# Kernel optimization log

Hardware: AMD Instinct MI355X
Metric: run time of the kernel (lower is better)

## Reference

```python
import jax, jax.numpy as jnp
import numpy as np
from jax.scipy.stats import norm

B, T = 64, 1024
RNN_DIM, EMB_DIM, ATTN_DIM = 1024, 512, 128
N_FILT, KSIZE, N_MEAN = 32, 31, 8
LOGVAR_MIN = float(np.log(0.1 ** 2))
LOGVAR_MAX = float(np.log(36.77 ** 2))


def setup_inputs() -> dict:
    key = jax.random.key(0)
    ks = jax.random.split(key, 10)
    return {
        "attention_hidden_state": jax.random.normal(ks[0], (B, RNN_DIM), jnp.float32),
        "memory": jax.random.normal(ks[1], (B, T, EMB_DIM), jnp.float32),
        "processed_memory": jax.random.normal(ks[2], (B, T, ATTN_DIM), jnp.float32),
        "attention_weights_cat": jax.random.uniform(ks[3], (B, 2, T), jnp.float32),
        "prev_means": jnp.zeros((B,), jnp.float32),
        "mask": jnp.zeros((B, T), bool),
        # learned parameters (all Linear layers bias=False; conv bias=False)
        "W_query": jax.random.normal(ks[4], (ATTN_DIM, RNN_DIM), jnp.float32) * 0.02,
        "conv_w": jax.random.normal(ks[5], (N_FILT, 2, KSIZE), jnp.float32) * 0.1,
        "W_loc": jax.random.normal(ks[6], (ATTN_DIM, N_FILT), jnp.float32) * 0.1,
        "W_mean": jax.random.normal(ks[7], (N_MEAN, ATTN_DIM), jnp.float32) * 0.05,
        "W_logvar": jax.random.normal(ks[8], (1, ATTN_DIM), jnp.float32) * 0.05,
    }


def reference(attention_hidden_state, memory, processed_memory, attention_weights_cat,
              prev_means, mask, W_query, conv_w, W_loc, W_mean, W_logvar):
    pad = (KSIZE - 1) // 2
    # query projection: [B, 1, attn_dim]
    processed_query = (attention_hidden_state @ W_query.T)[:, None, :]
    # location layer: conv1d(2 -> n_filters, same padding) then dense -> [B, T, attn_dim]
    loc = jax.lax.conv_general_dilated(
        attention_weights_cat, conv_w, window_strides=(1,),
        padding=[(pad, pad)], dimension_numbers=("NCH", "OIH", "NCH"))  # [B, F, T]
    processed_loc = jnp.einsum("bft,df->btd", loc, W_loc)
    pred = jnp.tanh(processed_query + processed_loc + processed_memory)  # [B, T, D]
    avg = pred.mean(axis=1)                                              # [B, D]
    # monotonic mean increment (soft_clip = softplus, keeps increments positive)
    mean_inc = jax.nn.softplus(avg @ W_mean.T).sum(axis=-1)              # [B]
    means = prev_means + mean_inc                                        # [B]
    logvars = (LOGVAR_MAX - LOGVAR_MIN) * jax.nn.sigmoid(avg @ W_logvar.T) + LOGVAR_MIN
    stds = jnp.exp(0.5 * logvars[:, 0])                                  # [B]
    # Gaussian window: CDF(x+0.5) - CDF(x-0.5), x = 0..T-1
    x = jnp.arange(T, dtype=jnp.float32)[None, :]                        # [1, T]
    mu, sd = means[:, None], stds[:, None]
    p = norm.cdf((x + 0.5 - mu) / sd) - norm.cdf((x - 0.5 - mu) / sd)    # [B, T]
    attention_weights = jnp.where(mask, 0.0, p)
    attention_context = jnp.einsum("bt,bte->be", attention_weights, memory)
    return attention_context, attention_weights
```

## Files before the change

### kernel.cpp

```cpp
#include <hip/hip_runtime.h>
#include <math.h>

#define B 64
#define T 1024
#define RNN_DIM 1024
#define EMB_DIM 512
#define ATTN_DIM 128
#define N_FILT 32
#define KSIZE 31
#define N_MEAN 8

#define LOGVAR_MIN (-4.605170185988091f)
#define LOGVAR_MAX (7.2093654f)

#define TTILE 256
#define AWWIN 288
#define MAGIC 0x73C0FFEEu

typedef __attribute__((ext_vector_type(8))) short bf16x8;
typedef __attribute__((ext_vector_type(4))) float f32x4;

__device__ __forceinline__ unsigned short f2bf(float x) {
    unsigned u = __float_as_uint(x);
    u += 0x7FFFu + ((u >> 16) & 1u);
    return (unsigned short)(u >> 16);
}

__global__ __launch_bounds__(512, 1) void fused_kernel(
        const float* __restrict__ hidden,
        const float* __restrict__ memory,
        const float* __restrict__ pm,
        const float* __restrict__ awcat,
        const float* __restrict__ prevm,
        const unsigned char* __restrict__ mask,
        const float* __restrict__ Wq,
        const float* __restrict__ convw,
        const float* __restrict__ Wloc,
        const float* __restrict__ Wmean,
        const float* __restrict__ Wlogvar,
        unsigned* __restrict__ pqflags,
        unsigned* __restrict__ avgflags,
        float* __restrict__ pq_ws,
        float* __restrict__ avg_part,
        float* __restrict__ out_ctx,
        float* __restrict__ out_w) {
    __shared__ __align__(16) float aw_s[2][AWWIN];
    __shared__ __align__(16) float pq_s[ATTN_DIM];
    __shared__ __align__(16) unsigned short loc_bf[TTILE * 32];
    __shared__ __align__(16) unsigned short wl_bf[ATTN_DIM * 32];
    __shared__ __align__(16) float red2[8][ATTN_DIM];
    __shared__ __align__(16) float a_s[ATTN_DIM];
    __shared__ float w_s[T];
    __shared__ __align__(16) float4 cred_s[16][32];
    __shared__ float musd_s[2];
    __shared__ int slo_s[8], shi_s[8];

    const int x = blockIdx.x;
    const int b = blockIdx.y;
    const int tid = threadIdx.x;
    const int t0 = x * TTILE;
    const int lane = tid & 63;
    const int w = tid >> 6;

    for (int idx = tid; idx < 2 * AWWIN; idx += 512) {
        int c = idx / AWWIN, j = idx - c * AWWIN;
        int tg = t0 - 16 + j;
        aw_s[c][j] = (tg >= 0 && tg < T) ? awcat[(size_t)b * 2 * T + c * T + tg] : 0.f;
    }

    {
        const float4* wsrc = (const float4*)Wloc;
        float4 v0 = wsrc[tid * 2], v1 = wsrc[tid * 2 + 1];
        uint4 pk;
        pk.x = (unsigned)f2bf(v0.x) | ((unsigned)f2bf(v0.y) << 16);
        pk.y = (unsigned)f2bf(v0.z) | ((unsigned)f2bf(v0.w) << 16);
        pk.z = (unsigned)f2bf(v1.x) | ((unsigned)f2bf(v1.y) << 16);
        pk.w = (unsigned)f2bf(v1.z) | ((unsigned)f2bf(v1.w) << 16);
        *(uint4*)&wl_bf[tid * 8] = pk;
    }

    {
        const float4* h4 = (const float4*)(hidden + (size_t)b * RNN_DIM);
        float4 hv0 = h4[lane], hv1 = h4[lane + 64];
        float4 hv2 = h4[lane + 128], hv3 = h4[lane + 192];
#pragma unroll
        for (int pass = 0; pass < 4; ++pass) {
            int d = x * 32 + pass * 8 + w;
            const float4* w4 = (const float4*)(Wq + (size_t)d * RNN_DIM);
            float4 wa = w4[lane], wb = w4[lane + 64];
            float4 wc = w4[lane + 128], wd = w4[lane + 192];
            float acc = hv0.x * wa.x + hv0.y * wa.y + hv0.z * wa.z + hv0.w * wa.w;
            acc += hv1.x * wb.x + hv1.y * wb.y + hv1.z * wb.z + hv1.w * wb.w;
            acc += hv2.x * wc.x + hv2.y * wc.y + hv2.z * wc.z + hv2.w * wc.w;
            acc += hv3.x * wd.x + hv3.y * wd.y + hv3.z * wd.z + hv3.w * wd.w;
#pragma unroll
            for (int off = 32; off > 0; off >>= 1)
                acc += __shfl_xor(acc, off, 64);
            if (lane == 0)
                __hip_atomic_store(&pq_ws[b * ATTN_DIM + d], acc,
                                   __ATOMIC_RELAXED, __HIP_MEMORY_SCOPE_AGENT);
        }
        asm volatile("s_waitcnt vmcnt(0)" ::: "memory");
    }
    __syncthreads();
    if (tid == 0)
        __hip_atomic_store(&pqflags[b * 4 + x], MAGIC,
                           __ATOMIC_RELEASE, __HIP_MEMORY_SCOPE_AGENT);

    {
        int f = tid & 31, tg8 = tid >> 5;
        float cw0[KSIZE], cw1[KSIZE];
#pragma unroll
        for (int k = 0; k < KSIZE; ++k) {
            cw0[k] = convw[(f * 2 + 0) * KSIZE + k];
            cw1[k] = convw[(f * 2 + 1) * KSIZE + k];
        }
#pragma unroll
        for (int p = 0; p < 2; ++p) {
            int o = tg8 + 16 * p;
            float a0[40], a1[40];
#pragma unroll
            for (int j = 0; j < 10; ++j) {
                float4 v0 = *(const float4*)&aw_s[0][o * 8 + 4 * j];
                float4 v1 = *(const float4*)&aw_s[1][o * 8 + 4 * j];
                a0[4 * j] = v0.x; a0[4 * j + 1] = v0.y; a0[4 * j + 2] = v0.z; a0[4 * j + 3] = v0.w;
                a1[4 * j] = v1.x; a1[4 * j + 1] = v1.y; a1[4 * j + 2] = v1.z; a1[4 * j + 3] = v1.w;
            }
#pragma unroll
            for (int i = 0; i < 8; ++i) {
                float s = 0.f;
#pragma unroll
                for (int k = 0; k < KSIZE; ++k)
                    s += a0[i + k + 1] * cw0[k] + a1[i + k + 1] * cw1[k];
                loc_bf[(o * 8 + i) * 32 + f] = f2bf(s);
            }
        }
    }
    __syncthreads();

    if (tid == 0) {
#pragma unroll
        for (int s = 0; s < 4; ++s) {
            const unsigned* fp = &pqflags[b * 4 + s];
            while (__hip_atomic_load(fp, __ATOMIC_RELAXED, __HIP_MEMORY_SCOPE_AGENT) != MAGIC)
                __builtin_amdgcn_s_sleep(1);
        }
    }
    __syncthreads();
    if (tid < ATTN_DIM)
        pq_s[tid] = __hip_atomic_load(&pq_ws[b * ATTN_DIM + tid],
                                      __ATOMIC_RELAXED, __HIP_MEMORY_SCOPE_AGENT);
    __syncthreads();

    {
        int col = lane & 15;
        int kg = lane >> 4;
        const float* pmL = pm + (size_t)(b * T + t0 + w * 32) * ATTN_DIM + col;

        float pmr[2][8][4];
#pragma unroll
        for (int m = 0; m < 2; ++m)
#pragma unroll
            for (int n = 0; n < 8; ++n)
#pragma unroll
                for (int j = 0; j < 4; ++j)
                    pmr[m][n][j] = pmL[(size_t)(m * 16 + kg * 4 + j) * ATTN_DIM + n * 16];

        bf16x8 bfrag[8];
#pragma unroll
        for (int n = 0; n < 8; ++n)
            bfrag[n] = *(const bf16x8*)&wl_bf[(n * 16 + col) * 32 + kg * 8];
        bf16x8 af[2];
#pragma unroll
        for (int m = 0; m < 2; ++m)
            af[m] = *(const bf16x8*)&loc_bf[(w * 32 + m * 16 + col) * 32 + kg * 8];
        float pqv[8];
#pragma unroll
        for (int n = 0; n < 8; ++n) pqv[n] = pq_s[n * 16 + col];

        float accs[8];
#pragma unroll
        for (int n = 0; n < 8; ++n) accs[n] = 0.f;
#pragma unroll
        for (int m = 0; m < 2; ++m) {
#pragma unroll
            for (int n = 0; n < 8; ++n) {
                f32x4 c = {0.f, 0.f, 0.f, 0.f};
                c = __builtin_amdgcn_mfma_f32_16x16x32_bf16(af[m], bfrag[n], c, 0, 0, 0);
#pragma unroll
                for (int j = 0; j < 4; ++j) {
                    float xv = c[j] + pqv[n] + pmr[m][n][j];
                    float e = __expf(2.f * xv);
                    accs[n] += 1.f - 2.f / (e + 1.f);
                }
            }
        }
#pragma unroll
        for (int n = 0; n < 8; ++n) {
            float s = accs[n];
            s += __shfl_xor(s, 16, 64);
            s += __shfl_xor(s, 32, 64);
            if (lane < 16) red2[w][n * 16 + lane] = s;
        }
    }
    __syncthreads();

    if (tid < ATTN_DIM) {
        float s = 0.f;
#pragma unroll
        for (int w2 = 0; w2 < 8; ++w2) s += red2[w2][tid];
        __hip_atomic_store(&avg_part[((size_t)b * 4 + x) * ATTN_DIM + tid], s,
                           __ATOMIC_RELAXED, __HIP_MEMORY_SCOPE_AGENT);
    }
    asm volatile("s_waitcnt vmcnt(0)" ::: "memory");
    __syncthreads();
    if (tid == 0) {
        __hip_atomic_store(&avgflags[b * 4 + x], MAGIC,
                           __ATOMIC_RELEASE, __HIP_MEMORY_SCOPE_AGENT);
#pragma unroll
        for (int s = 0; s < 4; ++s) {
            const unsigned* fp = &avgflags[b * 4 + s];
            while (__hip_atomic_load(fp, __ATOMIC_RELAXED, __HIP_MEMORY_SCOPE_AGENT) != MAGIC)
                __builtin_amdgcn_s_sleep(1);
        }
    }
    __syncthreads();

    if (tid < ATTN_DIM) {
        float s = 0.f;
#pragma unroll
        for (int ss = 0; ss < 4; ++ss)
            s += __hip_atomic_load(&avg_part[((size_t)b * 4 + ss) * ATTN_DIM + tid],
                                   __ATOMIC_RELAXED, __HIP_MEMORY_SCOPE_AGENT);
        a_s[tid] = s * (1.f / (float)T);
    }
    __syncthreads();

    if (tid < 64) {
        float macc[N_MEAN];
#pragma unroll
        for (int m = 0; m < N_MEAN; ++m) macc[m] = 0.f;
        float lv = 0.f;
#pragma unroll
        for (int i = 0; i < 2; ++i) {
            int d = tid + i * 64;
            float a = a_s[d];
#pragma unroll
            for (int m = 0; m < N_MEAN; ++m) macc[m] += a * Wmean[m * ATTN_DIM + d];
            lv += a * Wlogvar[d];
        }
#pragma unroll
        for (int off = 32; off > 0; off >>= 1) {
#pragma unroll
            for (int m = 0; m < N_MEAN; ++m) macc[m] += __shfl_xor(macc[m], off, 64);
            lv += __shfl_xor(lv, off, 64);
        }
        if (tid == 0) {
            float mean_inc = 0.f;
#pragma unroll
            for (int m = 0; m < N_MEAN; ++m) {
                float xx = macc[m];
                mean_inc += fmaxf(xx, 0.f) + log1pf(expf(-fabsf(xx)));
            }
            float mu = prevm[b] + mean_inc;
            float sig = 1.f / (1.f + expf(-lv));
            float logvar = (LOGVAR_MAX - LOGVAR_MIN) * sig + LOGVAR_MIN;
            musd_s[0] = mu;
            musd_s[1] = 1.f / expf(0.5f * logvar);
        }
    }
    __syncthreads();

    float mu = musd_s[0];
    float rsd = musd_s[1];
    const float is2 = 0.7071067811865476f;
    int lo = T, hi = -1;
#pragma unroll
    for (int r = 0; r < 2; ++r) {
        int t = tid + r * 512;
        float z1 = ((float)t + 0.5f - mu) * rsd * is2;
        float z2 = ((float)t - 0.5f - mu) * rsd * is2;
        float p = 0.5f * (erff(z1) - erff(z2));
        if (mask[(size_t)b * T + t]) p = 0.f;
        w_s[t] = p;
        if ((t >> 8) == x) out_w[(size_t)b * T + t] = p;
        if (p != 0.f) { lo = min(lo, t); hi = max(hi, t); }
    }
#pragma unroll
    for (int off = 32; off > 0; off >>= 1) {
        lo = min(lo, __shfl_xor(lo, off, 64));
        hi = max(hi, __shfl_xor(hi, off, 64));
    }
    if (lane == 0) { slo_s[w] = lo; shi_s[w] = hi; }
    __syncthreads();
#pragma unroll
    for (int wv = 0; wv < 8; ++wv) {
        lo = min(lo, slo_s[wv]);
        hi = max(hi, shi_s[wv]);
    }

    {
        int e4 = x * 32 + (tid & 31);
        int trow = tid >> 5;
        const float4* m4 = (const float4*)memory + (size_t)b * T * (EMB_DIM / 4);
        float4 acc = make_float4(0.f, 0.f, 0.f, 0.f);
        for (int t = lo + trow; t <= hi; t += 16) {
            float wvv = w_s[t];
            float4 mm = m4[(size_t)t * (EMB_DIM / 4) + e4];
            acc.x += wvv * mm.x;
            acc.y += wvv * mm.y;
            acc.z += wvv * mm.z;
            acc.w += wvv * mm.w;
        }
        if (trow != 0) cred_s[trow][tid & 31] = acc;
        __syncthreads();
        if (trow == 0) {
#pragma unroll
            for (int r = 1; r < 16; ++r) {
                float4 o = cred_s[r][tid & 31];
                acc.x += o.x; acc.y += o.y; acc.z += o.z; acc.w += o.w;
            }
            ((float4*)(out_ctx + (size_t)b * EMB_DIM))[e4] = acc;
        }
    }
}

extern "C" void kernel_launch(void* const* d_in, const int* in_sizes, int n_in,
                              void* d_out, int out_size, void* d_ws, size_t ws_size,
                              hipStream_t stream) {
    const float* hidden  = (const float*)d_in[0];
    const float* memory  = (const float*)d_in[1];
    const float* pm      = (const float*)d_in[2];
    const float* awcat   = (const float*)d_in[3];
    const float* prevm   = (const float*)d_in[4];
    const unsigned char* mask = (const unsigned char*)d_in[5];
    const float* Wq      = (const float*)d_in[6];
    const float* convw   = (const float*)d_in[7];
    const float* Wloc    = (const float*)d_in[8];
    const float* Wmean   = (const float*)d_in[9];
    const float* Wlogvar = (const float*)d_in[10];

    unsigned* pqflags  = (unsigned*)d_ws;
    unsigned* avgflags = pqflags + 256;
    float* pq_ws       = (float*)d_ws + 512;
    float* avg_part    = pq_ws + B * ATTN_DIM;

    float* out_ctx = (float*)d_out;
    float* out_w   = out_ctx + B * EMB_DIM;

    fused_kernel<<<dim3(4, B), 512, 0, stream>>>(
        hidden, memory, pm, awcat, prevm, mask, Wq, convw, Wloc, Wmean,
        Wlogvar, pqflags, avgflags, pq_ws, avg_part, out_ctx, out_w);
}
```

Baseline: 33.44 us.

## Split each batch over eight blocks of 128 timesteps instead of four

Doubles the grid to 8 blocks per batch row (512 total), each covering 128 timesteps, 16 query dims and 64 embedding columns. Launch bounds now allow 4 blocks per CU. The conv is restructured to process one channel at a time, which lowers register pressure. The pq flag wait is moved after the pm/fragment loads so the wait overlaps with memory traffic. The cross-block spin barriers now wait on 8 flags, and the context reduction becomes a tree. The goal is more parallelism and occupancy on the many-CU GPU. The cost is extra sync overhead and redundant per-block work such as the window computation and the W_loc conversion.

```diff
diff --git a/kernel.cpp b/kernel.cpp
--- a/kernel.cpp
+++ b/kernel.cpp
@@ -13,8 +13,9 @@
 #define LOGVAR_MIN (-4.605170185988091f)
 #define LOGVAR_MAX (7.2093654f)
 
-#define TTILE 256
-#define AWWIN 288
+#define NX 8
+#define TTILE 128
+#define AWWIN 160
 #define MAGIC 0x73C0FFEEu
 
 typedef __attribute__((ext_vector_type(8))) short bf16x8;
@@ -26,7 +27,7 @@
     return (unsigned short)(u >> 16);
 }
 
-__global__ __launch_bounds__(512, 1) void fused_kernel(
+__global__ __launch_bounds__(512, 4) void fused_kernel(
         const float* __restrict__ hidden,
         const float* __restrict__ memory,
         const float* __restrict__ pm,
@@ -51,12 +52,12 @@
     __shared__ __align__(16) float red2[8][ATTN_DIM];
     __shared__ __align__(16) float a_s[ATTN_DIM];
     __shared__ float w_s[T];
-    __shared__ __align__(16) float4 cred_s[16][32];
+    __shared__ __align__(16) float4 cred_s[32][16];
     __shared__ float musd_s[2];
     __shared__ int slo_s[8], shi_s[8];
 
-    const int x = blockIdx.x;
-    const int b = blockIdx.y;
+    const int b = blockIdx.x;
+    const int x = blockIdx.y;
     const int tid = threadIdx.x;
     const int t0 = x * TTILE;
     const int lane = tid & 63;
@@ -84,8 +85,8 @@
         float4 hv0 = h4[lane], hv1 = h4[lane + 64];
         float4 hv2 = h4[lane + 128], hv3 = h4[lane + 192];
 #pragma unroll
-        for (int pass = 0; pass < 4; ++pass) {
-            int d = x * 32 + pass * 8 + w;
+        for (int pass = 0; pass < 2; ++pass) {
+            int d = x * 16 + pass * 8 + w;
             const float4* w4 = (const float4*)(Wq + (size_t)d * RNN_DIM);
             float4 wa = w4[lane], wb = w4[lane + 64];
             float4 wc = w4[lane + 128], wd = w4[lane + 192];
@@ -104,76 +105,73 @@
     }
     __syncthreads();
     if (tid == 0)
-        __hip_atomic_store(&pqflags[b * 4 + x], MAGIC,
+        __hip_atomic_store(&pqflags[b * NX + x], MAGIC,
                            __ATOMIC_RELEASE, __HIP_MEMORY_SCOPE_AGENT);
 
     {
-        int f = tid & 31, tg8 = tid >> 5;
-        float cw0[KSIZE], cw1[KSIZE];
-#pragma unroll
-        for (int k = 0; k < KSIZE; ++k) {
-            cw0[k] = convw[(f * 2 + 0) * KSIZE + k];
-            cw1[k] = convw[(f * 2 + 1) * KSIZE + k];
-        }
-#pragma unroll
-        for (int p = 0; p < 2; ++p) {
-            int o = tg8 + 16 * p;
-            float a0[40], a1[40];
+        int f = tid & 31, o = tid >> 5;
+        float s[8];
+#pragma unroll
+        for (int i = 0; i < 8; ++i) s[i] = 0.f;
+#pragma unroll
+        for (int c = 0; c < 2; ++c) {
+            float cw[KSIZE];
+#pragma unroll
+            for (int k = 0; k < KSIZE; ++k)
+                cw[k] = convw[f * 2 * KSIZE + c * KSIZE + k];
+            float a[40];
 #pragma unroll
             for (int j = 0; j < 10; ++j) {
-                float4 v0 = *(const float4*)&aw_s[0][o * 8 + 4 * j];
-                float4 v1 = *(const float4*)&aw_s[1][o * 8 + 4 * j];
-                a0[4 * j] = v0.x; a0[4 * j + 1] = v0.y; a0[4 * j + 2] = v0.z; a0[4 * j + 3] = v0.w;
-                a1[4 * j] = v1.x; a1[4 * j + 1] = v1.y; a1[4 * j + 2] = v1.z; a1[4 * j + 3] = v1.w;
+                float4 v = *(const float4*)&aw_s[c][o * 8 + 4 * j];
+                a[4 * j] = v.x; a[4 * j + 1] = v.y; a[4 * j + 2] = v.z; a[4 * j + 3] = v.w;
             }
 #pragma unroll
             for (int i = 0; i < 8; ++i) {
-                float s = 0.f;
+                float t = 0.f;
 #pragma unroll
                 for (int k = 0; k < KSIZE; ++k)
-                    s += a0[i + k + 1] * cw0[k] + a1[i + k + 1] * cw1[k];
-                loc_bf[(o * 8 + i) * 32 + f] = f2bf(s);
-            }
-        }
-    }
-    __syncthreads();
-
-    if (tid == 0) {
-#pragma unroll
-        for (int s = 0; s < 4; ++s) {
-            const unsigned* fp = &pqflags[b * 4 + s];
-            while (__hip_atomic_load(fp, __ATOMIC_RELAXED, __HIP_MEMORY_SCOPE_AGENT) != MAGIC)
-                __builtin_amdgcn_s_sleep(1);
-        }
-    }
-    __syncthreads();
-    if (tid < ATTN_DIM)
-        pq_s[tid] = __hip_atomic_load(&pq_ws[b * ATTN_DIM + tid],
-                                      __ATOMIC_RELAXED, __HIP_MEMORY_SCOPE_AGENT);
+                    t += a[i + k + 1] * cw[k];
+                s[i] += t;
+            }
+        }
+#pragma unroll
+        for (int i = 0; i < 8; ++i)
+            loc_bf[(o * 8 + i) * 32 + f] = f2bf(s[i]);
+    }
     __syncthreads();
 
     {
         int col = lane & 15;
         int kg = lane >> 4;
-        const float* pmL = pm + (size_t)(b * T + t0 + w * 32) * ATTN_DIM + col;
-
-        float pmr[2][8][4];
-#pragma unroll
-        for (int m = 0; m < 2; ++m)
-#pragma unroll
-            for (int n = 0; n < 8; ++n)
-#pragma unroll
-                for (int j = 0; j < 4; ++j)
-                    pmr[m][n][j] = pmL[(size_t)(m * 16 + kg * 4 + j) * ATTN_DIM + n * 16];
+        const float* pmL = pm + (size_t)(b * T + t0 + w * 16) * ATTN_DIM + col;
+
+        float pmr[8][4];
+#pragma unroll
+        for (int n = 0; n < 8; ++n)
+#pragma unroll
+            for (int j = 0; j < 4; ++j)
+                pmr[n][j] = pmL[(size_t)(kg * 4 + j) * ATTN_DIM + n * 16];
 
         bf16x8 bfrag[8];
 #pragma unroll
         for (int n = 0; n < 8; ++n)
             bfrag[n] = *(const bf16x8*)&wl_bf[(n * 16 + col) * 32 + kg * 8];
-        bf16x8 af[2];
-#pragma unroll
-        for (int m = 0; m < 2; ++m)
-            af[m] = *(const bf16x8*)&loc_bf[(w * 32 + m * 16 + col) * 32 + kg * 8];
+        bf16x8 af = *(const bf16x8*)&loc_bf[(w * 16 + col) * 32 + kg * 8];
+
+        if (tid == 0) {
+#pragma unroll
+            for (int s = 0; s < NX; ++s) {
+                const unsigned* fp = &pqflags[b * NX + s];
+                while (__hip_atomic_load(fp, __ATOMIC_RELAXED, __HIP_MEMORY_SCOPE_AGENT) != MAGIC)
+                    __builtin_amdgcn_s_sleep(1);
+            }
+        }
+        __syncthreads();
+        if (tid < ATTN_DIM)
+            pq_s[tid] = __hip_atomic_load(&pq_ws[b * ATTN_DIM + tid],
+                                          __ATOMIC_RELAXED, __HIP_MEMORY_SCOPE_AGENT);
+        __syncthreads();
+
         float pqv[8];
 #pragma unroll
         for (int n = 0; n < 8; ++n) pqv[n] = pq_s[n * 16 + col];
@@ -182,17 +180,14 @@
 #pragma unroll
         for (int n = 0; n < 8; ++n) accs[n] = 0.f;
 #pragma unroll
-        for (int m = 0; m < 2; ++m) {
-#pragma unroll
-            for (int n = 0; n < 8; ++n) {
-                f32x4 c = {0.f, 0.f, 0.f, 0.f};
-                c = __builtin_amdgcn_mfma_f32_16x16x32_bf16(af[m], bfrag[n], c, 0, 0, 0);
-#pragma unroll
-                for (int j = 0; j < 4; ++j) {
-                    float xv = c[j] + pqv[n] + pmr[m][n][j];
-                    float e = __expf(2.f * xv);
-                    accs[n] += 1.f - 2.f / (e + 1.f);
-                }
+        for (int n = 0; n < 8; ++n) {
+            f32x4 c = {0.f, 0.f, 0.f, 0.f};
+            c = __builtin_amdgcn_mfma_f32_16x16x32_bf16(af, bfrag[n], c, 0, 0, 0);
+#pragma unroll
+            for (int j = 0; j < 4; ++j) {
+                float xv = c[j] + pqv[n] + pmr[n][j];
+                float e = __expf(2.f * xv);
+                accs[n] += 1.f - 2.f / (e + 1.f);
             }
         }
 #pragma unroll
@@ -209,17 +204,17 @@
         float s = 0.f;
 #pragma unroll
         for (int w2 = 0; w2 < 8; ++w2) s += red2[w2][tid];
-        __hip_atomic_store(&avg_part[((size_t)b * 4 + x) * ATTN_DIM + tid], s,
+        __hip_atomic_store(&avg_part[((size_t)b * NX + x) * ATTN_DIM + tid], s,
                            __ATOMIC_RELAXED, __HIP_MEMORY_SCOPE_AGENT);
     }
     asm volatile("s_waitcnt vmcnt(0)" ::: "memory");
     __syncthreads();
     if (tid == 0) {
-        __hip_atomic_store(&avgflags[b * 4 + x], MAGIC,
+        __hip_atomic_store(&avgflags[b * NX + x], MAGIC,
                            __ATOMIC_RELEASE, __HIP_MEMORY_SCOPE_AGENT);
 #pragma unroll
-        for (int s = 0; s < 4; ++s) {
-            const unsigned* fp = &avgflags[b * 4 + s];
+        for (int s = 0; s < NX; ++s) {
+            const unsigned* fp = &avgflags[b * NX + s];
             while (__hip_atomic_load(fp, __ATOMIC_RELAXED, __HIP_MEMORY_SCOPE_AGENT) != MAGIC)
                 __builtin_amdgcn_s_sleep(1);
         }
@@ -229,8 +224,8 @@
     if (tid < ATTN_DIM) {
         float s = 0.f;
 #pragma unroll
-        for (int ss = 0; ss < 4; ++ss)
-            s += __hip_atomic_load(&avg_part[((size_t)b * 4 + ss) * ATTN_DIM + tid],
+        for (int ss = 0; ss < NX; ++ss)
+            s += __hip_atomic_load(&avg_part[((size_t)b * NX + ss) * ATTN_DIM + tid],
                                    __ATOMIC_RELAXED, __HIP_MEMORY_SCOPE_AGENT);
         a_s[tid] = s * (1.f / (float)T);
     }
@@ -283,7 +278,7 @@
         float p = 0.5f * (erff(z1) - erff(z2));
         if (mask[(size_t)b * T + t]) p = 0.f;
         w_s[t] = p;
-        if ((t >> 8) == x) out_w[(size_t)b * T + t] = p;
+        if ((t >> 7) == x) out_w[(size_t)b * T + t] = p;
         if (p != 0.f) { lo = min(lo, t); hi = max(hi, t); }
     }
 #pragma unroll
@@ -300,11 +295,12 @@
     }
 
     {
-        int e4 = x * 32 + (tid & 31);
-        int trow = tid >> 5;
+        int e = tid & 15;
+        int e4 = x * 16 + e;
+        int trow = tid >> 4;
         const float4* m4 = (const float4*)memory + (size_t)b * T * (EMB_DIM / 4);
         float4 acc = make_float4(0.f, 0.f, 0.f, 0.f);
-        for (int t = lo + trow; t <= hi; t += 16) {
+        for (int t = lo + trow; t <= hi; t += 32) {
             float wvv = w_s[t];
             float4 mm = m4[(size_t)t * (EMB_DIM / 4) + e4];
             acc.x += wvv * mm.x;
@@ -312,16 +308,21 @@
             acc.z += wvv * mm.z;
             acc.w += wvv * mm.w;
         }
-        if (trow != 0) cred_s[trow][tid & 31] = acc;
+        cred_s[trow][e] = acc;
         __syncthreads();
-        if (trow == 0) {
-#pragma unroll
-            for (int r = 1; r < 16; ++r) {
-                float4 o = cred_s[r][tid & 31];
-                acc.x += o.x; acc.y += o.y; acc.z += o.z; acc.w += o.w;
-            }
-            ((float4*)(out_ctx + (size_t)b * EMB_DIM))[e4] = acc;
-        }
+#pragma unroll
+        for (int step = 16; step >= 1; step >>= 1) {
+            if (trow < step) {
+                float4 o = cred_s[trow + step][e];
+                cred_s[trow][e].x += o.x;
+                cred_s[trow][e].y += o.y;
+                cred_s[trow][e].z += o.z;
+                cred_s[trow][e].w += o.w;
+            }
+            __syncthreads();
+        }
+        if (tid < 16)
+            ((float4*)(out_ctx + (size_t)b * EMB_DIM))[e4] = cred_s[0][e];
     }
 }
 
@@ -341,14 +342,14 @@
     const float* Wlogvar = (const float*)d_in[10];
 
     unsigned* pqflags  = (unsigned*)d_ws;
-    unsigned* avgflags = pqflags + 256;
-    float* pq_ws       = (float*)d_ws + 512;
+    unsigned* avgflags = pqflags + B * NX;
+    float* pq_ws       = (float*)d_ws + 1024;
     float* avg_part    = pq_ws + B * ATTN_DIM;
 
     float* out_ctx = (float*)d_out;
     float* out_w   = out_ctx + B * EMB_DIM;
 
-    fused_kernel<<<dim3(4, B), 512, 0, stream>>>(
+    fused_kernel<<<dim3(B, NX), 512, 0, stream>>>(
         hidden, memory, pm, awcat, prevm, mask, Wq, convw, Wloc, Wmean,
         Wlogvar, pqflags, avgflags, pq_ws, avg_part, out_ctx, out_w);
 }
```

New measurement: 34.35 us. 2.7% more time.

## Vectorize processed-memory loads via permuted column mapping, defer query-flag wait, fast tanh

Applied to the files above, without the earlier changes.

Remaps the MFMA output columns so each lane owns 8 contiguous attention dims, which lets processed_memory be read with float4 loads instead of strided scalar loads. To keep results consistent, the bf16 W_loc rows, the pq index and the reduction index are permuted to match. The spin-wait on the query-projection flags now runs after the fragment loads, so those loads can overlap the wait. tanh now uses hardware exp2 and rcp intrinsics, trading a little accuracy for fewer instructions.

```diff
diff --git a/kernel.cpp b/kernel.cpp
--- a/kernel.cpp
+++ b/kernel.cpp
@@ -16,6 +16,7 @@
 #define TTILE 256
 #define AWWIN 288
 #define MAGIC 0x73C0FFEEu
+#define TWO_LOG2E 2.8853900817779268f
 
 typedef __attribute__((ext_vector_type(8))) short bf16x8;
 typedef __attribute__((ext_vector_type(4))) float f32x4;
@@ -24,6 +25,11 @@
     unsigned u = __float_as_uint(x);
     u += 0x7FFFu + ((u >> 16) & 1u);
     return (unsigned short)(u >> 16);
+}
+
+__device__ __forceinline__ float fast_tanh(float x) {
+    float e = __builtin_amdgcn_exp2f(x * TWO_LOG2E);
+    return 1.f - 2.f * __builtin_amdgcn_rcpf(e + 1.f);
 }
 
 __global__ __launch_bounds__(512, 1) void fused_kernel(
@@ -69,14 +75,16 @@
     }
 
     {
-        const float4* wsrc = (const float4*)Wloc;
-        float4 v0 = wsrc[tid * 2], v1 = wsrc[tid * 2 + 1];
+        int d = tid >> 2, seg = tid & 3;
+        const float4* wsrc = (const float4*)Wloc + tid * 2;
+        float4 v0 = wsrc[0], v1 = wsrc[1];
         uint4 pk;
         pk.x = (unsigned)f2bf(v0.x) | ((unsigned)f2bf(v0.y) << 16);
         pk.y = (unsigned)f2bf(v0.z) | ((unsigned)f2bf(v0.w) << 16);
         pk.z = (unsigned)f2bf(v1.x) | ((unsigned)f2bf(v1.y) << 16);
         pk.w = (unsigned)f2bf(v1.z) | ((unsigned)f2bf(v1.w) << 16);
-        *(uint4*)&wl_bf[tid * 8] = pk;
+        int prow = (d & 7) * 16 + (d >> 3);
+        *(uint4*)&wl_bf[prow * 32 + seg * 8] = pk;
     }
 
     {
@@ -138,33 +146,25 @@
     }
     __syncthreads();
 
-    if (tid == 0) {
-#pragma unroll
-        for (int s = 0; s < 4; ++s) {
-            const unsigned* fp = &pqflags[b * 4 + s];
-            while (__hip_atomic_load(fp, __ATOMIC_RELAXED, __HIP_MEMORY_SCOPE_AGENT) != MAGIC)
-                __builtin_amdgcn_s_sleep(1);
-        }
-    }
-    __syncthreads();
-    if (tid < ATTN_DIM)
-        pq_s[tid] = __hip_atomic_load(&pq_ws[b * ATTN_DIM + tid],
-                                      __ATOMIC_RELAXED, __HIP_MEMORY_SCOPE_AGENT);
-    __syncthreads();
-
     {
         int col = lane & 15;
         int kg = lane >> 4;
-        const float* pmL = pm + (size_t)(b * T + t0 + w * 32) * ATTN_DIM + col;
-
-        float pmr[2][8][4];
+
+        float pmr[2][4][8];
 #pragma unroll
         for (int m = 0; m < 2; ++m)
 #pragma unroll
-            for (int n = 0; n < 8; ++n)
-#pragma unroll
-                for (int j = 0; j < 4; ++j)
-                    pmr[m][n][j] = pmL[(size_t)(m * 16 + kg * 4 + j) * ATTN_DIM + n * 16];
+            for (int j = 0; j < 4; ++j) {
+                const float* rowp = pm
+                    + (size_t)(b * T + t0 + w * 32 + m * 16 + kg * 4 + j) * ATTN_DIM
+                    + col * 8;
+                float4 v0 = *(const float4*)rowp;
+                float4 v1 = *(const float4*)(rowp + 4);
+                pmr[m][j][0] = v0.x; pmr[m][j][1] = v0.y;
+                pmr[m][j][2] = v0.z; pmr[m][j][3] = v0.w;
+                pmr[m][j][4] = v1.x; pmr[m][j][5] = v1.y;
+                pmr[m][j][6] = v1.z; pmr[m][j][7] = v1.w;
+            }
 
         bf16x8 bfrag[8];
 #pragma unroll
@@ -174,9 +174,24 @@
 #pragma unroll
         for (int m = 0; m < 2; ++m)
             af[m] = *(const bf16x8*)&loc_bf[(w * 32 + m * 16 + col) * 32 + kg * 8];
+
+        if (tid == 0) {
+#pragma unroll
+            for (int s = 0; s < 4; ++s) {
+                const unsigned* fp = &pqflags[b * 4 + s];
+                while (__hip_atomic_load(fp, __ATOMIC_RELAXED, __HIP_MEMORY_SCOPE_AGENT) != MAGIC)
+                    __builtin_amdgcn_s_sleep(1);
+            }
+        }
+        __syncthreads();
+        if (tid < ATTN_DIM)
+            pq_s[tid] = __hip_atomic_load(&pq_ws[b * ATTN_DIM + tid],
+                                          __ATOMIC_RELAXED, __HIP_MEMORY_SCOPE_AGENT);
+        __syncthreads();
+
         float pqv[8];
 #pragma unroll
-        for (int n = 0; n < 8; ++n) pqv[n] = pq_s[n * 16 + col];
+        for (int n = 0; n < 8; ++n) pqv[n] = pq_s[col * 8 + n];
 
         float accs[8];
 #pragma unroll
@@ -188,11 +203,8 @@
                 f32x4 c = {0.f, 0.f, 0.f, 0.f};
                 c = __builtin_amdgcn_mfma_f32_16x16x32_bf16(af[m], bfrag[n], c, 0, 0, 0);
 #pragma unroll
-                for (int j = 0; j < 4; ++j) {
-                    float xv = c[j] + pqv[n] + pmr[m][n][j];
-                    float e = __expf(2.f * xv);
-                    accs[n] += 1.f - 2.f / (e + 1.f);
-                }
+                for (int j = 0; j < 4; ++j)
+                    accs[n] += fast_tanh(c[j] + pqv[n] + pmr[m][j][n]);
             }
         }
 #pragma unroll
@@ -200,7 +212,7 @@
             float s = accs[n];
             s += __shfl_xor(s, 16, 64);
             s += __shfl_xor(s, 32, 64);
-            if (lane < 16) red2[w][n * 16 + lane] = s;
+            if (lane < 16) red2[w][lane * 8 + n] = s;
         }
     }
     __syncthreads();
@@ -300,7 +312,8 @@
     }
 
     {
-        int e4 = x * 32 + (tid & 31);
+        int e = tid & 31;
+        int e4 = x * 32 + e;
         int trow = tid >> 5;
         const float4* m4 = (const float4*)memory + (size_t)b * T * (EMB_DIM / 4);
         float4 acc = make_float4(0.f, 0.f, 0.f, 0.f);
@@ -312,12 +325,12 @@
             acc.z += wvv * mm.z;
             acc.w += wvv * mm.w;
         }
-        if (trow != 0) cred_s[trow][tid & 31] = acc;
+        if (trow != 0) cred_s[trow][e] = acc;
         __syncthreads();
         if (trow == 0) {
 #pragma unroll
             for (int r = 1; r < 16; ++r) {
-                float4 o = cred_s[r][tid & 31];
+                float4 o = cred_s[r][e];
                 acc.x += o.x; acc.y += o.y; acc.z += o.z; acc.w += o.w;
             }
             ((float4*)(out_ctx + (size_t)b * EMB_DIM))[e4] = acc;
```

Result: faster. 31.19 us (-6.7%).
